# Performance work log

Measured on AMD Instinct MI355X. Metric: run time of the kernel, lower is better.

Reference implementation:

```python
import jax, jax.numpy as jnp
import numpy as np

D = 256   # dim = vis_dim = key_channels = value_channels = audio_dim
BT = 64   # batch*time
H = 64
W = 64
L = 32    # audio length

_CONV_NAMES = ["vis_project", "av", "vv", "vo", "ao", "vs_key", "vs_q1", "vs_q2",
               "as_key", "as_q1", "as_q2", "outconv", "aoc"]


def _conv1(x, w, b):
    # pointwise Conv1d: x [B,C,Lx], w [O,C], b [O]
    return jnp.einsum('oc,bcl->bol', w, x) + b[None, :, None]


def _inorm(x, eps=1e-5):
    # InstanceNorm1d (affine=False): normalize over last (spatial) axis
    m = jnp.mean(x, axis=-1, keepdims=True)
    v = jnp.var(x, axis=-1, keepdims=True)
    return (x - m) * jax.lax.rsqrt(v + eps)


def _gelu(x):
    return jax.nn.gelu(x, approximate=False)


def setup_inputs() -> dict:
    key = jax.random.key(0)
    ks = jax.random.split(key, 40)
    inp = {
        "x": jax.random.normal(ks[0], (BT, D, H, W), jnp.float32),
        "audio": jax.random.normal(ks[1], (BT, D, L), jnp.float32),
        "audio_mask": jnp.ones((BT, L, 1), jnp.float32),
    }
    for i, n in enumerate(_CONV_NAMES):
        inp[n + "_w"] = jax.random.normal(ks[3 + 2 * i], (D, D), jnp.float32) * 0.05
        inp[n + "_b"] = jax.random.normal(ks[4 + 2 * i], (D,), jnp.float32) * 0.01
    inp["gate_w1"] = jax.random.normal(ks[30], (D, D), jnp.float32) * 0.05
    inp["gate_w2"] = jax.random.normal(ks[31], (D, D), jnp.float32) * 0.05
    inp["vis_weight"] = jnp.ones((1,), jnp.float32)
    inp["audio_weight"] = jnp.ones((1,), jnp.float32)
    return inp


def reference(x, audio, audio_mask,
              vis_project_w, vis_project_b, av_w, av_b, vv_w, vv_b, vo_w, vo_b,
              ao_w, ao_b, vs_key_w, vs_key_b, vs_q1_w, vs_q1_b, vs_q2_w, vs_q2_b,
              as_key_w, as_key_b, as_q1_w, as_q1_b, as_q2_w, as_q2_b,
              outconv_w, outconv_b, aoc_w, aoc_b, gate_w1, gate_w2,
              vis_weight, audio_weight):
    bt, c, h, w = x.shape
    hw = h * w
    xf = x.reshape(bt, c, hw)                       # [BT,C,HW] (channels-first tokens)
    scale = float(D) ** -0.5                         # key_channels ** -0.5
    maskT = jnp.swapaxes(audio_mask, 1, 2)           # [BT,1,L]

    # vis_project (Conv1d 1x1 + GELU)
    vis = _gelu(_conv1(xf, vis_project_w, vis_project_b))       # [BT,C,HW]

    # ---- AV_Interaction ----
    audio_value = _conv1(audio, av_w, av_b) * maskT              # [BT,C,L]

    # Visual_Sim (kernel=1 -> unfold is identity)
    q1 = _inorm(_conv1(xf, vs_q1_w, vs_q1_b))                    # [BT,C,HW]
    q = _inorm(_conv1(q1, vs_q2_w, vs_q2_b))                     # [BT,C,HW]
    k = _conv1(audio, vs_key_w, vs_key_b) * maskT                # [BT,C,L]
    sim_v = jnp.einsum('bch,bcl->bhl', q, k) * scale             # [BT,HW,L]
    sim_v = sim_v + (10000.0 * maskT - 10000.0)                  # mask keys
    sim_v = jax.nn.softmax(sim_v, axis=-1)
    vw = jax.nn.softmax(vis_weight)[0]                           # softmax over size-1 -> 1.0
    vis_out = jnp.einsum('bhl,bcl->bhc', sim_v * vw, audio_value)  # [BT,HW,C]
    vis_out = _inorm(_conv1(jnp.swapaxes(vis_out, 1, 2), vo_w, vo_b))  # [BT,C,HW]

    # Audio_Sim (kernel=(1,1) -> pad/unfold identity)
    aq = _conv1(_conv1(audio, as_q1_w, as_q1_b), as_q2_w, as_q2_b)  # [BT,C,L]
    ak = _inorm(_conv1(xf, as_key_w, as_key_b))                     # [BT,C,HW]
    aqT = jnp.swapaxes(aq, 1, 2) * audio_mask                       # [BT,L,C]
    sim_a = jnp.einsum('blc,bch->blh', aqT, ak) * scale             # [BT,L,HW]
    sim_a = sim_a + (10000.0 * audio_mask - 10000.0)                # mask query rows
    sim_a = jax.nn.softmax(sim_a, axis=-1)
    aw = jax.nn.softmax(audio_weight)[0]
    vis_value = _inorm(_conv1(xf, vv_w, vv_b))                      # [BT,C,HW]
    audio_o = jnp.einsum('blh,bch->blc', sim_a * aw, vis_value)     # [BT,L,C]
    audio_res = _conv1(jnp.swapaxes(audio_o, 1, 2), ao_w, ao_b)     # [BT,C,L]

    # ---- Dual fusion: vis * vis_weight_map, out_conv ----
    vis = _gelu(_conv1(vis * vis_out, outconv_w, outconv_b))        # [BT,C,HW]
    vis_res = jnp.swapaxes(vis, 1, 2)                               # [BT,HW,C]

    # ---- DAM block: gated residual + audio residual ----
    gate = jnp.tanh(jax.nn.relu(vis_res @ gate_w1.T) @ gate_w2.T)   # [BT,HW,C]
    x_tok = jnp.swapaxes(xf, 1, 2) + gate * vis_res                 # [BT,HW,C]
    x_out = jnp.swapaxes(x_tok, 1, 2).reshape(bt, c, h, w)
    audio_out = audio + _gelu(_conv1(audio_res, aoc_w, aoc_b))      # [BT,C,L]
    return (x_out, audio_out)
```

## Files before the change

### kernel.cpp

```cpp
#include <hip/hip_runtime.h>
#include <math.h>

#define BT 64
#define CH 256
#define HW 4096
#define AL 32
#define SCALE 0.0625f

typedef unsigned short ushort_t;
typedef __bf16 bf16x8 __attribute__((ext_vector_type(8)));
typedef short  short8 __attribute__((ext_vector_type(8)));
typedef float  f32x4  __attribute__((ext_vector_type(4)));

__device__ __forceinline__ float gelu_f(float x){
    return 0.5f*x*(1.0f+erff(x*0.70710678118654752f));
}
__device__ __forceinline__ ushort_t f2bf(float f){
    unsigned int u = __builtin_bit_cast(unsigned int, f);
    u += 0x7fffu + ((u>>16)&1u);
    return (ushort_t)(u>>16);
}
__device__ __forceinline__ float bf2f(ushort_t h){
    unsigned int u = ((unsigned int)h)<<16;
    return __builtin_bit_cast(float, u);
}

#define GLOAD_LDS16(gp, lp) __builtin_amdgcn_global_load_lds( \
    (const __attribute__((address_space(1))) unsigned int*)(gp), \
    (__attribute__((address_space(3))) unsigned int*)(lp), 16, 0, 0)

template<int EPI, int TOUT>
__global__ __launch_bounds__(256,2)
void gemm_mfma_kernel(const ushort_t* __restrict__ Wb, const float* __restrict__ bias,
                      const ushort_t* __restrict__ Xt, float* __restrict__ Out,
                      ushort_t* __restrict__ OutB,
                      const float* __restrict__ E1, const float* __restrict__ E2)
{
    __shared__ ushort_t sW[128*32];
    __shared__ ushort_t sX[128*32];
    const int b  = blockIdx.z;
    const int o0 = blockIdx.y*128, p0 = blockIdx.x*128;
    const int tid = threadIdx.x, lane = tid & 63, w = tid >> 6;
    const int wm = w >> 1, wn = w & 1;
    const int rr = lane >> 2;
    const int kk8 = (lane & 3) * 8;

    f32x4 acc[4][4] = {};

    for (int k0 = 0; k0 < CH; k0 += 32) {
        #pragma unroll
        for (int j = 0; j < 2; ++j) {
            const ushort_t* gw = Wb + (size_t)(o0 + w*32 + j*16 + rr)*CH + k0 + kk8;
            GLOAD_LDS16(gw, sW + (size_t)w*1024 + j*512);
        }
        #pragma unroll
        for (int j = 0; j < 2; ++j) {
            const ushort_t* gx = Xt + ((size_t)b*HW + p0 + w*32 + j*16 + rr)*CH + k0 + kk8;
            GLOAD_LDS16(gx, sX + (size_t)w*1024 + j*512);
        }
        __syncthreads();
        bf16x8 af[4], bfr[4];
        #pragma unroll
        for (int mt = 0; mt < 4; ++mt) {
            short8 raw = *(const short8*)(sW + (size_t)(wm*64 + mt*16 + (lane&15))*32 + (lane>>4)*8);
            af[mt] = __builtin_bit_cast(bf16x8, raw);
        }
        #pragma unroll
        for (int nt = 0; nt < 4; ++nt) {
            short8 raw = *(const short8*)(sX + (size_t)(wn*64 + nt*16 + (lane&15))*32 + (lane>>4)*8);
            bfr[nt] = __builtin_bit_cast(bf16x8, raw);
        }
        #pragma unroll
        for (int mt = 0; mt < 4; ++mt)
            #pragma unroll
            for (int nt = 0; nt < 4; ++nt)
                acc[mt][nt] = __builtin_amdgcn_mfma_f32_16x16x32_bf16(af[mt], bfr[nt], acc[mt][nt], 0, 0, 0);
        __syncthreads();
    }

    const int pcol = lane & 15, quad = lane >> 4;
    const size_t obase = (size_t)b*CH*HW;
    if (TOUT == 0) {
        #pragma unroll
        for (int mt = 0; mt < 4; ++mt) {
            #pragma unroll
            for (int r = 0; r < 4; ++r) {
                const int o = o0 + wm*64 + mt*16 + quad*4 + r;
                const float bv = bias ? bias[o] : 0.0f;
                #pragma unroll
                for (int nt = 0; nt < 4; ++nt) {
                    const int p = p0 + wn*64 + nt*16 + pcol;
                    float v = acc[mt][nt][r] + bv;
                    if (EPI == 1) v = gelu_f(v);
                    if (EPI == 2) v = fmaxf(v, 0.0f);
                    if (EPI == 3) {
                        const size_t idx = obase + (size_t)o*HW + p;
                        v = E1[idx] + tanhf(v)*E2[idx];
                    }
                    Out[obase + (size_t)o*HW + p] = v;
                }
            }
        }
    } else {
        #pragma unroll
        for (int mt = 0; mt < 4; ++mt) {
            const int ob = o0 + wm*64 + mt*16 + quad*4;
            #pragma unroll
            for (int nt = 0; nt < 4; ++nt) {
                const int p = p0 + wn*64 + nt*16 + pcol;
                ushort4 u;
                float v0 = acc[mt][nt][0] + (bias ? bias[ob+0] : 0.f);
                float v1 = acc[mt][nt][1] + (bias ? bias[ob+1] : 0.f);
                float v2 = acc[mt][nt][2] + (bias ? bias[ob+2] : 0.f);
                float v3 = acc[mt][nt][3] + (bias ? bias[ob+3] : 0.f);
                if (EPI == 1) { v0=gelu_f(v0); v1=gelu_f(v1); v2=gelu_f(v2); v3=gelu_f(v3); }
                if (EPI == 2) { v0=fmaxf(v0,0.f); v1=fmaxf(v1,0.f); v2=fmaxf(v2,0.f); v3=fmaxf(v3,0.f); }
                u.x=f2bf(v0); u.y=f2bf(v1); u.z=f2bf(v2); u.w=f2bf(v3);
                *(ushort4*)(OutB + ((size_t)b*HW + p)*CH + ob) = u;
            }
        }
    }
}

template<int MODE>
__global__ __launch_bounds__(256)
void transpose_bf16_kernel(const float* __restrict__ Xa, const ushort_t* __restrict__ Mul,
                           ushort_t* __restrict__ Out)
{
    __shared__ float sT[32][33];
    const int b = blockIdx.z, c0 = blockIdx.y*32, p0 = blockIdx.x*32;
    const int tid = threadIdx.x;
    {
        const int cr = tid >> 3, pq = (tid & 7)*4;
        const float4 v = *(const float4*)(Xa + ((size_t)b*CH + c0 + cr)*HW + p0 + pq);
        sT[cr][pq+0]=v.x; sT[cr][pq+1]=v.y; sT[cr][pq+2]=v.z; sT[cr][pq+3]=v.w;
    }
    __syncthreads();
    {
        const int pr = tid >> 3, cq = (tid & 7)*4;
        const size_t oidx = ((size_t)b*HW + p0 + pr)*CH + c0 + cq;
        float v0 = sT[cq+0][pr], v1 = sT[cq+1][pr], v2 = sT[cq+2][pr], v3 = sT[cq+3][pr];
        if (MODE == 1) {
            const ushort4 m = *(const ushort4*)(Mul + oidx);
            v0 *= bf2f(m.x); v1 *= bf2f(m.y); v2 *= bf2f(m.z); v3 *= bf2f(m.w);
        }
        ushort4 u; u.x=f2bf(v0); u.y=f2bf(v1); u.z=f2bf(v2); u.w=f2bf(v3);
        *(ushort4*)(Out + oidx) = u;
    }
}

__global__ __launch_bounds__(256)
void wconv_kernel(const float* w0, const float* w1, const float* w2, const float* w3,
                  const float* w4, const float* w5, const float* w6, const float* w7,
                  const float* w8, ushort_t* __restrict__ Wb)
{
    const float* src;
    switch (blockIdx.y) {
        case 0: src=w0; break; case 1: src=w1; break; case 2: src=w2; break;
        case 3: src=w3; break; case 4: src=w4; break; case 5: src=w5; break;
        case 6: src=w6; break; case 7: src=w7; break; default: src=w8; break;
    }
    const int i = (blockIdx.x*256 + threadIdx.x)*4;
    const float4 v = *(const float4*)(src + i);
    ushort4 u; u.x=f2bf(v.x); u.y=f2bf(v.y); u.z=f2bf(v.z); u.w=f2bf(v.w);
    *(ushort4*)(Wb + (size_t)blockIdx.y*65536 + i) = u;
}

__global__ __launch_bounds__(256)
void inorm_hw_kernel(float* __restrict__ Buf)
{
    const size_t base = (size_t)blockIdx.x * HW;
    const int tid = threadIdx.x;
    float4 v[4];
    float s=0.f, ss=0.f;
    #pragma unroll
    for (int i=0;i<4;++i){
        v[i] = *(const float4*)(Buf + base + tid*4 + i*1024);
        s  += v[i].x+v[i].y+v[i].z+v[i].w;
        ss += v[i].x*v[i].x + v[i].y*v[i].y + v[i].z*v[i].z + v[i].w*v[i].w;
    }
    #pragma unroll
    for (int off=1; off<64; off<<=1){
        s  += __shfl_xor(s, off);
        ss += __shfl_xor(ss, off);
    }
    __shared__ float rs[4], rss[4];
    if ((tid&63)==0){ rs[tid>>6]=s; rss[tid>>6]=ss; }
    __syncthreads();
    s  = rs[0]+rs[1]+rs[2]+rs[3];
    ss = rss[0]+rss[1]+rss[2]+rss[3];
    const float mean = s * (1.0f/HW);
    const float var  = ss * (1.0f/HW) - mean*mean;
    const float r = rsqrtf(var + 1e-5f);
    #pragma unroll
    for (int i=0;i<4;++i){
        float4 t;
        t.x=(v[i].x-mean)*r; t.y=(v[i].y-mean)*r; t.z=(v[i].z-mean)*r; t.w=(v[i].w-mean)*r;
        *(float4*)(Buf + base + tid*4 + i*1024) = t;
    }
}

template<int EPI>
__global__ __launch_bounds__(256)
void conv_l_kernel(const float* __restrict__ W, const float* __restrict__ bias,
                   const float* __restrict__ X, float* __restrict__ Out,
                   const float* __restrict__ Mask, const float* __restrict__ Resid)
{
    const int b = blockIdx.x;
    const int o = blockIdx.y*8 + (threadIdx.x>>5);
    const int l = threadIdx.x & 31;
    const float* xb = X + (size_t)b*CH*AL + l;
    const float* wr = W + (size_t)o*CH;
    float acc = bias ? bias[o] : 0.0f;
    #pragma unroll 8
    for (int c=0;c<CH;++c) acc = fmaf(wr[c], xb[(size_t)c*AL], acc);
    const size_t oi = (size_t)b*CH*AL + (size_t)o*AL + l;
    if (EPI==1) acc *= Mask[b*AL + l];
    if (EPI==2) acc = Resid[oi] + gelu_f(acc);
    Out[oi] = acc;
}

__global__ __launch_bounds__(256)
void attn_v_kernel(const float* __restrict__ Q, const float* __restrict__ K,
                   const float* __restrict__ AV, const float* __restrict__ Mask,
                   float* __restrict__ Out)
{
    __shared__ float smem[12288];
    __shared__ float sBias[32];
    const int b  = blockIdx.y;
    const int p0 = blockIdx.x * 64;
    const int tid = threadIdx.x;
    const int p = tid & 63, lg = tid >> 6;

    {
        const float* kb = K + (size_t)b*CH*AL;
        #pragma unroll
        for (int i=0;i<32;++i) smem[tid + 256*i] = kb[tid + 256*i];
        if (tid < 32) sBias[tid] = 10000.f*Mask[b*AL+tid] - 10000.f;
    }
    float s[8] = {0.f,0.f,0.f,0.f,0.f,0.f,0.f,0.f};
    const float* qb = Q + (size_t)b*CH*HW + p0;
    for (int c0=0; c0<CH; c0+=64){
        __syncthreads();
        #pragma unroll
        for (int i=0;i<4;++i){
            const int cc = (tid>>4) + 16*i;
            const int pp = (tid&15)*4;
            *(float4*)&smem[8192 + cc*64 + pp] = *(const float4*)(qb + (size_t)(c0+cc)*HW + pp);
        }
        __syncthreads();
        for (int cc=0; cc<64; ++cc){
            const float qv = smem[8192 + cc*64 + p];
            const float* kr = &smem[(c0+cc)*32 + lg*8];
            #pragma unroll
            for (int j=0;j<8;++j) s[j] = fmaf(qv, kr[j], s[j]);
        }
    }
    __syncthreads();
    #pragma unroll
    for (int j=0;j<8;++j) smem[8192 + p*33 + lg*8 + j] = s[j]*SCALE + sBias[lg*8+j];
    {
        const float* avb = AV + (size_t)b*CH*AL;
        #pragma unroll
        for (int i=0;i<32;++i) smem[tid + 256*i] = avb[tid + 256*i];
    }
    __syncthreads();
    if (tid < 64){
        float* row = &smem[8192 + tid*33];
        float m = row[0];
        #pragma unroll
        for (int l=1;l<32;++l) m = fmaxf(m, row[l]);
        float z = 0.f;
        #pragma unroll
        for (int l=0;l<32;++l){ const float e = expf(row[l]-m); row[l]=e; z+=e; }
        const float rz = 1.f/z;
        #pragma unroll
        for (int l=0;l<32;++l) row[l] *= rz;
    }
    __syncthreads();
    float w[32];
    #pragma unroll
    for (int l=0;l<32;++l) w[l] = smem[8192 + p*33 + l];
    float* ob = Out + (size_t)b*CH*HW + p0 + p;
    for (int ci=0; ci<64; ++ci){
        const int c = lg*64 + ci;
        const float* ar = &smem[c*32];
        float acc = 0.f;
        #pragma unroll
        for (int l=0;l<32;++l) acc = fmaf(w[l], ar[l], acc);
        ob[(size_t)c*HW] = acc;
    }
}

__global__ __launch_bounds__(256)
void sima_raw_kernel(const float* __restrict__ AQ, const float* __restrict__ AK,
                     const float* __restrict__ Mask, float* __restrict__ Sraw)
{
    __shared__ float sAQ[CH*AL];
    const int b = blockIdx.y;
    const int p = blockIdx.x*256 + threadIdx.x;
    const int tid = threadIdx.x;
    #pragma unroll
    for (int i=0;i<32;++i){
        const int idx = tid + 256*i;
        sAQ[idx] = AQ[(size_t)b*CH*AL + idx] * Mask[b*AL + (idx&31)] * SCALE;
    }
    __syncthreads();
    float s[32];
    #pragma unroll
    for (int l=0;l<32;++l) s[l]=0.f;
    const float* akb = AK + (size_t)b*CH*HW + p;
    for (int c=0;c<CH;++c){
        const float a = akb[(size_t)c*HW];
        const float* qr = &sAQ[c*32];
        #pragma unroll
        for (int l=0;l<32;++l) s[l] = fmaf(qr[l], a, s[l]);
    }
    float* outp = Sraw + (size_t)b*AL*HW + p;
    #pragma unroll
    for (int l=0;l<32;++l) outp[(size_t)l*HW] = s[l];
}

__global__ __launch_bounds__(256)
void sima_stats_kernel(const float* __restrict__ Sraw, float2* __restrict__ Stats)
{
    const size_t base = (size_t)blockIdx.x * HW;
    const int tid = threadIdx.x;
    float v[16];
    #pragma unroll
    for (int i=0;i<4;++i){
        const float4 t = *(const float4*)(Sraw + base + tid*4 + i*1024);
        v[i*4+0]=t.x; v[i*4+1]=t.y; v[i*4+2]=t.z; v[i*4+3]=t.w;
    }
    float m = v[0];
    #pragma unroll
    for (int i=1;i<16;++i) m = fmaxf(m, v[i]);
    #pragma unroll
    for (int off=1; off<64; off<<=1) m = fmaxf(m, __shfl_xor(m, off));
    __shared__ float rm[4], rz[4];
    if ((tid&63)==0) rm[tid>>6]=m;
    __syncthreads();
    m = fmaxf(fmaxf(rm[0],rm[1]), fmaxf(rm[2],rm[3]));
    float z=0.f;
    #pragma unroll
    for (int i=0;i<16;++i) z += expf(v[i]-m);
    #pragma unroll
    for (int off=1; off<64; off<<=1) z += __shfl_xor(z, off);
    if ((tid&63)==0) rz[tid>>6]=z;
    __syncthreads();
    if (tid==0) Stats[blockIdx.x] = make_float2(m, 1.0f/(rz[0]+rz[1]+rz[2]+rz[3]));
}

__global__ __launch_bounds__(256)
void sima_pv_kernel(const float* __restrict__ Sraw, const float2* __restrict__ Stats,
                    const float* __restrict__ VV, float* __restrict__ AO)
{
    __shared__ float sA[32*33];
    __shared__ float sB[64*36];
    __shared__ float sM[32], sR[32];
    const int b  = blockIdx.x >> 2;
    const int c0 = (blockIdx.x & 3) * 64;
    const int tid = threadIdx.x;
    if (tid < 32){
        const float2 st = Stats[b*AL + tid];
        sM[tid] = st.x; sR[tid] = st.y;
    }
    __syncthreads();
    const int lh = tid & 15;
    const int cq = tid >> 4;
    const int lr = tid >> 3, k4 = (tid & 7) * 4;
    float acc[2][4] = {{0.f,0.f,0.f,0.f},{0.f,0.f,0.f,0.f}};
    for (int p0=0; p0<HW; p0+=32){
        {
            const float4 t = *(const float4*)(Sraw + ((size_t)b*AL + lr)*HW + p0 + k4);
            const float mm = sM[lr], rr2 = sR[lr];
            sA[lr*33 + k4+0] = expf(t.x-mm)*rr2;
            sA[lr*33 + k4+1] = expf(t.y-mm)*rr2;
            sA[lr*33 + k4+2] = expf(t.z-mm)*rr2;
            sA[lr*33 + k4+3] = expf(t.w-mm)*rr2;
        }
        #pragma unroll
        for (int i=0;i<2;++i){
            const int cc = (tid>>3) + 32*i;
            *(float4*)&sB[cc*36 + k4] = *(const float4*)(VV + ((size_t)b*CH + c0 + cc)*HW + p0 + k4);
        }
        __syncthreads();
        #pragma unroll
        for (int kk=0;kk<32;++kk){
            const float a0 = sA[lh*33 + kk];
            const float a1 = sA[(lh+16)*33 + kk];
            #pragma unroll
            for (int j=0;j<4;++j){
                const float bb = sB[(cq*4+j)*36 + kk];
                acc[0][j] = fmaf(a0, bb, acc[0][j]);
                acc[1][j] = fmaf(a1, bb, acc[1][j]);
            }
        }
        __syncthreads();
    }
    #pragma unroll
    for (int j=0;j<4;++j){
        AO[((size_t)b*CH + c0 + cq*4 + j)*AL + lh]      = acc[0][j];
        AO[((size_t)b*CH + c0 + cq*4 + j)*AL + lh + 16] = acc[1][j];
    }
}

extern "C" void kernel_launch(void* const* d_in, const int* in_sizes, int n_in,
                              void* d_out, int out_size, void* d_ws, size_t ws_size,
                              hipStream_t stream)
{
    (void)in_sizes; (void)n_in; (void)out_size; (void)ws_size;
    const float* x     = (const float*)d_in[0];
    const float* audio = (const float*)d_in[1];
    const float* amask = (const float*)d_in[2];
    const float* vis_project_w = (const float*)d_in[3];
    const float* vis_project_b = (const float*)d_in[4];
    const float* av_w = (const float*)d_in[5];
    const float* av_b = (const float*)d_in[6];
    const float* vv_w = (const float*)d_in[7];
    const float* vv_b = (const float*)d_in[8];
    const float* vo_w = (const float*)d_in[9];
    const float* vo_b = (const float*)d_in[10];
    const float* ao_w = (const float*)d_in[11];
    const float* ao_b = (const float*)d_in[12];
    const float* vs_key_w = (const float*)d_in[13];
    const float* vs_key_b = (const float*)d_in[14];
    const float* vs_q1_w = (const float*)d_in[15];
    const float* vs_q1_b = (const float*)d_in[16];
    const float* vs_q2_w = (const float*)d_in[17];
    const float* vs_q2_b = (const float*)d_in[18];
    const float* as_key_w = (const float*)d_in[19];
    const float* as_key_b = (const float*)d_in[20];
    const float* as_q1_w = (const float*)d_in[21];
    const float* as_q1_b = (const float*)d_in[22];
    const float* as_q2_w = (const float*)d_in[23];
    const float* as_q2_b = (const float*)d_in[24];
    const float* outconv_w = (const float*)d_in[25];
    const float* outconv_b = (const float*)d_in[26];
    const float* aoc_w = (const float*)d_in[27];
    const float* aoc_b = (const float*)d_in[28];
    const float* gate_w1 = (const float*)d_in[29];
    const float* gate_w2 = (const float*)d_in[30];

    float* out_x = (float*)d_out;
    float* out_a = out_x + (size_t)BT*CH*HW;
    float* B     = out_x;

    const size_t BIG = (size_t)BT*CH*HW;
    ushort_t* Xt   = (ushort_t*)d_ws;
    ushort_t* VISB = Xt + BIG;
    float*  A     = (float*)(VISB + BIG);
    float*  SIMA  = A + BIG;
    float2* STATS = (float2*)(SIMA + (size_t)BT*AL*HW);
    float*  S0 = (float*)(STATS + BT*AL);
    float*  S1 = S0 + (size_t)BT*CH*AL;
    float*  S2 = S1 + (size_t)BT*CH*AL;
    float*  S3 = S2 + (size_t)BT*CH*AL;
    float*  S4 = S3 + (size_t)BT*CH*AL;
    ushort_t* Wb = (ushort_t*)(S4 + (size_t)BT*CH*AL);

    dim3 b256(256);
    dim3 gW(64, 9);
    dim3 gL(BT, CH/8);
    dim3 gT(HW/32, CH/32, BT);
    dim3 gG(HW/128, CH/128, BT);
    dim3 gNorm(BT*CH);
    dim3 gAttnV(HW/64, BT);
    dim3 gSimA(HW/256, BT);

    #define WSLOT(i) (Wb + (size_t)(i)*65536)
    hipLaunchKernelGGL(wconv_kernel, gW, b256, 0, stream,
                       vs_q1_w, as_key_w, vv_w, vis_project_w, vs_q2_w, vo_w, outconv_w, gate_w1, gate_w2, Wb);
    hipLaunchKernelGGL((conv_l_kernel<1>), gL, b256, 0, stream, av_w, av_b, audio, S0, amask, nullptr);
    hipLaunchKernelGGL((conv_l_kernel<1>), gL, b256, 0, stream, vs_key_w, vs_key_b, audio, S1, amask, nullptr);
    hipLaunchKernelGGL((conv_l_kernel<0>), gL, b256, 0, stream, as_q1_w, as_q1_b, audio, S3, nullptr, nullptr);
    hipLaunchKernelGGL((conv_l_kernel<0>), gL, b256, 0, stream, as_q2_w, as_q2_b, S3, S2, nullptr, nullptr);
    hipLaunchKernelGGL((transpose_bf16_kernel<0>), gT, b256, 0, stream, x, nullptr, Xt);
    hipLaunchKernelGGL((gemm_mfma_kernel<0,0>), gG, b256, 0, stream, WSLOT(0), vs_q1_b, Xt, A, nullptr, nullptr, nullptr);
    hipLaunchKernelGGL(inorm_hw_kernel, gNorm, b256, 0, stream, A);
    hipLaunchKernelGGL((gemm_mfma_kernel<0,0>), gG, b256, 0, stream, WSLOT(1), as_key_b, Xt, B, nullptr, nullptr, nullptr);
    hipLaunchKernelGGL(inorm_hw_kernel, gNorm, b256, 0, stream, B);
    hipLaunchKernelGGL(sima_raw_kernel, gSimA, b256, 0, stream, S2, B, amask, SIMA);
    hipLaunchKernelGGL(sima_stats_kernel, dim3(BT*AL), b256, 0, stream, SIMA, STATS);
    hipLaunchKernelGGL((gemm_mfma_kernel<0,0>), gG, b256, 0, stream, WSLOT(2), vv_b, Xt, B, nullptr, nullptr, nullptr);
    hipLaunchKernelGGL(inorm_hw_kernel, gNorm, b256, 0, stream, B);
    hipLaunchKernelGGL(sima_pv_kernel, dim3(BT*4), b256, 0, stream, SIMA, STATS, B, S4);
    hipLaunchKernelGGL((conv_l_kernel<0>), gL, b256, 0, stream, ao_w, ao_b, S4, S3, nullptr, nullptr);
    hipLaunchKernelGGL((conv_l_kernel<2>), gL, b256, 0, stream, aoc_w, aoc_b, S3, out_a, nullptr, audio);
    hipLaunchKernelGGL((gemm_mfma_kernel<1,1>), gG, b256, 0, stream, WSLOT(3), vis_project_b, Xt, nullptr, VISB, nullptr, nullptr);
    hipLaunchKernelGGL((transpose_bf16_kernel<0>), gT, b256, 0, stream, A, nullptr, Xt);
    hipLaunchKernelGGL((gemm_mfma_kernel<0,0>), gG, b256, 0, stream, WSLOT(4), vs_q2_b, Xt, B, nullptr, nullptr, nullptr);
    hipLaunchKernelGGL(inorm_hw_kernel, gNorm, b256, 0, stream, B);
    hipLaunchKernelGGL(attn_v_kernel, gAttnV, b256, 0, stream, B, S1, S0, amask, A);
    hipLaunchKernelGGL((transpose_bf16_kernel<0>), gT, b256, 0, stream, A, nullptr, Xt);
    hipLaunchKernelGGL((gemm_mfma_kernel<0,0>), gG, b256, 0, stream, WSLOT(5), vo_b, Xt, B, nullptr, nullptr, nullptr);
    hipLaunchKernelGGL(inorm_hw_kernel, gNorm, b256, 0, stream, B);
    hipLaunchKernelGGL((transpose_bf16_kernel<1>), gT, b256, 0, stream, B, VISB, Xt);
    hipLaunchKernelGGL((gemm_mfma_kernel<1,0>), gG, b256, 0, stream, WSLOT(6), outconv_b, Xt, A, nullptr, nullptr, nullptr);
    hipLaunchKernelGGL((transpose_bf16_kernel<0>), gT, b256, 0, stream, A, nullptr, Xt);
    hipLaunchKernelGGL((gemm_mfma_kernel<2,0>), gG, b256, 0, stream, WSLOT(7), nullptr, Xt, B, nullptr, nullptr, nullptr);
    hipLaunchKernelGGL((transpose_bf16_kernel<0>), gT, b256, 0, stream, B, nullptr, Xt);
    hipLaunchKernelGGL((gemm_mfma_kernel<3,0>), gG, b256, 0, stream, WSLOT(8), nullptr, Xt, out_x, nullptr, x, A);
    #undef WSLOT
}
```

Measured before the change: 3.315 ms.

## Fuse instance-norm statistics into GEMM epilogues and fold normalization into consumers

```diff
diff --git a/kernel.cpp b/kernel.cpp
--- a/kernel.cpp
+++ b/kernel.cpp
@@ -29,12 +29,13 @@
     (const __attribute__((address_space(1))) unsigned int*)(gp), \
     (__attribute__((address_space(3))) unsigned int*)(lp), 16, 0, 0)
 
-template<int EPI, int TOUT>
+template<int EPI, int TOUT, int WSTAT>
 __global__ __launch_bounds__(256,2)
 void gemm_mfma_kernel(const ushort_t* __restrict__ Wb, const float* __restrict__ bias,
                       const ushort_t* __restrict__ Xt, float* __restrict__ Out,
                       ushort_t* __restrict__ OutB,
-                      const float* __restrict__ E1, const float* __restrict__ E2)
+                      const float* __restrict__ E1, const float* __restrict__ E2,
+                      float* __restrict__ St)
 {
     __shared__ ushort_t sW[128*32];
     __shared__ ushort_t sX[128*32];
@@ -101,7 +102,7 @@
                 }
             }
         }
-    } else {
+    } else if (TOUT == 1) {
         #pragma unroll
         for (int mt = 0; mt < 4; ++mt) {
             const int ob = o0 + wm*64 + mt*16 + quad*4;
@@ -119,20 +120,110 @@
                 *(ushort4*)(OutB + ((size_t)b*HW + p)*CH + ob) = u;
             }
         }
-    }
+    } else {
+        #pragma unroll
+        for (int mt = 0; mt < 4; ++mt) {
+            const int ob = o0 + wm*64 + mt*16 + quad*4;
+            #pragma unroll
+            for (int nt = 0; nt < 4; ++nt) {
+                const int p = p0 + wn*64 + nt*16 + pcol;
+                float v[4];
+                #pragma unroll
+                for (int r = 0; r < 4; ++r) {
+                    float t = acc[mt][nt][r] + (bias ? bias[ob+r] : 0.f);
+                    if (EPI == 1) t = gelu_f(t);
+                    if (EPI == 2) t = fmaxf(t, 0.f);
+                    v[r] = t;
+                    Out[obase + (size_t)(ob+r)*HW + p] = t;
+                }
+                ushort4 u;
+                u.x=f2bf(v[0]); u.y=f2bf(v[1]); u.z=f2bf(v[2]); u.w=f2bf(v[3]);
+                *(ushort4*)(OutB + ((size_t)b*HW + p)*CH + ob) = u;
+            }
+        }
+    }
+
+    if (WSTAT) {
+        float s1[4][4], s2[4][4];
+        #pragma unroll
+        for (int mt = 0; mt < 4; ++mt) {
+            #pragma unroll
+            for (int r = 0; r < 4; ++r) {
+                const int o = o0 + wm*64 + mt*16 + quad*4 + r;
+                const float bv = bias ? bias[o] : 0.0f;
+                float a = 0.f, q = 0.f;
+                #pragma unroll
+                for (int nt = 0; nt < 4; ++nt) {
+                    const float v = acc[mt][nt][r] + bv;
+                    a += v; q += v*v;
+                }
+                #pragma unroll
+                for (int off = 1; off < 16; off <<= 1) {
+                    a += __shfl_xor(a, off);
+                    q += __shfl_xor(q, off);
+                }
+                s1[mt][r] = a; s2[mt][r] = q;
+            }
+        }
+        float* red = (float*)sW;
+        __syncthreads();
+        if (wn == 0 && pcol == 0) {
+            #pragma unroll
+            for (int mt = 0; mt < 4; ++mt)
+                #pragma unroll
+                for (int r = 0; r < 4; ++r) {
+                    const int ol = wm*64 + mt*16 + quad*4 + r;
+                    red[ol*2] = s1[mt][r]; red[ol*2+1] = s2[mt][r];
+                }
+        }
+        __syncthreads();
+        if (wn == 1 && pcol == 0) {
+            #pragma unroll
+            for (int mt = 0; mt < 4; ++mt)
+                #pragma unroll
+                for (int r = 0; r < 4; ++r) {
+                    const int ol = wm*64 + mt*16 + quad*4 + r;
+                    const int o = o0 + ol;
+                    atomicAdd(&St[((size_t)b*CH + o)*2],   red[ol*2]   + s1[mt][r]);
+                    atomicAdd(&St[((size_t)b*CH + o)*2+1], red[ol*2+1] + s2[mt][r]);
+                }
+        }
+    }
+}
+
+__global__ __launch_bounds__(256)
+void zero_kernel(float* __restrict__ p)
+{
+    p[blockIdx.x*256 + threadIdx.x] = 0.f;
+}
+
+__global__ __launch_bounds__(256)
+void stats_finalize_kernel(float* __restrict__ St)
+{
+    const int row = blockIdx.x*256 + threadIdx.x;
+    const float s1 = St[(size_t)row*2], s2 = St[(size_t)row*2+1];
+    const float mean = s1 * (1.0f/HW);
+    const float var  = s2 * (1.0f/HW) - mean*mean;
+    St[(size_t)row*2]   = mean;
+    St[(size_t)row*2+1] = rsqrtf(var + 1e-5f);
 }
 
 template<int MODE>
 __global__ __launch_bounds__(256)
 void transpose_bf16_kernel(const float* __restrict__ Xa, const ushort_t* __restrict__ Mul,
-                           ushort_t* __restrict__ Out)
+                           const float* __restrict__ St, ushort_t* __restrict__ Out)
 {
     __shared__ float sT[32][33];
     const int b = blockIdx.z, c0 = blockIdx.y*32, p0 = blockIdx.x*32;
     const int tid = threadIdx.x;
     {
         const int cr = tid >> 3, pq = (tid & 7)*4;
-        const float4 v = *(const float4*)(Xa + ((size_t)b*CH + c0 + cr)*HW + p0 + pq);
+        float4 v = *(const float4*)(Xa + ((size_t)b*CH + c0 + cr)*HW + p0 + pq);
+        if (MODE >= 1) {
+            const float m = St[((size_t)b*CH + c0 + cr)*2];
+            const float r = St[((size_t)b*CH + c0 + cr)*2+1];
+            v.x = (v.x-m)*r; v.y = (v.y-m)*r; v.z = (v.z-m)*r; v.w = (v.w-m)*r;
+        }
         sT[cr][pq+0]=v.x; sT[cr][pq+1]=v.y; sT[cr][pq+2]=v.z; sT[cr][pq+3]=v.w;
     }
     __syncthreads();
@@ -140,7 +231,7 @@
         const int pr = tid >> 3, cq = (tid & 7)*4;
         const size_t oidx = ((size_t)b*HW + p0 + pr)*CH + c0 + cq;
         float v0 = sT[cq+0][pr], v1 = sT[cq+1][pr], v2 = sT[cq+2][pr], v3 = sT[cq+3][pr];
-        if (MODE == 1) {
+        if (MODE == 2) {
             const ushort4 m = *(const ushort4*)(Mul + oidx);
             v0 *= bf2f(m.x); v1 *= bf2f(m.y); v2 *= bf2f(m.z); v3 *= bf2f(m.w);
         }
@@ -166,45 +257,12 @@
     *(ushort4*)(Wb + (size_t)blockIdx.y*65536 + i) = u;
 }
 
-__global__ __launch_bounds__(256)
-void inorm_hw_kernel(float* __restrict__ Buf)
-{
-    const size_t base = (size_t)blockIdx.x * HW;
-    const int tid = threadIdx.x;
-    float4 v[4];
-    float s=0.f, ss=0.f;
-    #pragma unroll
-    for (int i=0;i<4;++i){
-        v[i] = *(const float4*)(Buf + base + tid*4 + i*1024);
-        s  += v[i].x+v[i].y+v[i].z+v[i].w;
-        ss += v[i].x*v[i].x + v[i].y*v[i].y + v[i].z*v[i].z + v[i].w*v[i].w;
-    }
-    #pragma unroll
-    for (int off=1; off<64; off<<=1){
-        s  += __shfl_xor(s, off);
-        ss += __shfl_xor(ss, off);
-    }
-    __shared__ float rs[4], rss[4];
-    if ((tid&63)==0){ rs[tid>>6]=s; rss[tid>>6]=ss; }
-    __syncthreads();
-    s  = rs[0]+rs[1]+rs[2]+rs[3];
-    ss = rss[0]+rss[1]+rss[2]+rss[3];
-    const float mean = s * (1.0f/HW);
-    const float var  = ss * (1.0f/HW) - mean*mean;
-    const float r = rsqrtf(var + 1e-5f);
-    #pragma unroll
-    for (int i=0;i<4;++i){
-        float4 t;
-        t.x=(v[i].x-mean)*r; t.y=(v[i].y-mean)*r; t.z=(v[i].z-mean)*r; t.w=(v[i].w-mean)*r;
-        *(float4*)(Buf + base + tid*4 + i*1024) = t;
-    }
-}
-
-template<int EPI>
+template<int EPI, int TR>
 __global__ __launch_bounds__(256)
 void conv_l_kernel(const float* __restrict__ W, const float* __restrict__ bias,
                    const float* __restrict__ X, float* __restrict__ Out,
-                   const float* __restrict__ Mask, const float* __restrict__ Resid)
+                   const float* __restrict__ Mask, const float* __restrict__ Resid,
+                   const float* __restrict__ St)
 {
     const int b = blockIdx.x;
     const int o = blockIdx.y*8 + (threadIdx.x>>5);
@@ -214,87 +272,154 @@
     float acc = bias ? bias[o] : 0.0f;
     #pragma unroll 8
     for (int c=0;c<CH;++c) acc = fmaf(wr[c], xb[(size_t)c*AL], acc);
-    const size_t oi = (size_t)b*CH*AL + (size_t)o*AL + l;
     if (EPI==1) acc *= Mask[b*AL + l];
-    if (EPI==2) acc = Resid[oi] + gelu_f(acc);
-    Out[oi] = acc;
-}
-
-__global__ __launch_bounds__(256)
-void attn_v_kernel(const float* __restrict__ Q, const float* __restrict__ K,
-                   const float* __restrict__ AV, const float* __restrict__ Mask,
-                   float* __restrict__ Out)
-{
-    __shared__ float smem[12288];
+    if (EPI==4) acc *= Mask[b*AL + l] * St[((size_t)b*CH + o)*2+1] * SCALE;
+    if (EPI==2) {
+        const size_t oi = (size_t)b*CH*AL + (size_t)o*AL + l;
+        acc = Resid[oi] + gelu_f(acc);
+    }
+    if (TR == 0) Out[(size_t)b*CH*AL + (size_t)o*AL + l] = acc;
+    else         Out[((size_t)b*AL + l)*CH + o] = acc;
+}
+
+__global__ __launch_bounds__(256)
+void lbias_kernel(const float* __restrict__ Kn, const float* __restrict__ St,
+                  float* __restrict__ Lb)
+{
+    const int b = blockIdx.x, tid = threadIdx.x;
+    const int l = tid & 31, g = tid >> 5;
+    float s = 0.f;
+    #pragma unroll 8
+    for (int cc=0; cc<32; ++cc){
+        const int c = g*32 + cc;
+        s += St[((size_t)b*CH + c)*2] * Kn[((size_t)b*CH + c)*AL + l];
+    }
+    __shared__ float red[8][32];
+    red[g][l] = s;
+    __syncthreads();
+    if (tid < 32){
+        float t = 0.f;
+        #pragma unroll
+        for (int gg=0; gg<8; ++gg) t += red[gg][tid];
+        Lb[b*AL + tid] = -t;
+    }
+}
+
+__device__ __forceinline__ void attn_loadq(f32x4 (&dst)[8], const float* Qb, int kc){
+    #pragma unroll
+    for (int kk=0;kk<8;++kk)
+        dst[kk] = *(const f32x4*)(Qb + (size_t)(kc*8+kk)*HW);
+}
+__device__ __forceinline__ void attn_fma(float (&s)[4][4], const f32x4 (&q)[8],
+                                         const float* sKV, int kc, int lq){
+    #pragma unroll
+    for (int kk=0;kk<8;++kk){
+        const f32x4 kv = *(const f32x4*)&sKV[(kc*8+kk)*32 + lq*4];
+        #pragma unroll
+        for (int i=0;i<4;++i)
+            #pragma unroll
+            for (int j=0;j<4;++j)
+                s[i][j] = fmaf(q[kk][i], kv[j], s[i][j]);
+    }
+}
+
+__global__ __launch_bounds__(256,3)
+void attn_v_kernel(const float* __restrict__ Q, const float* __restrict__ Kn,
+                   const float* __restrict__ AVt, const float* __restrict__ Lb,
+                   const float* __restrict__ Mask, ushort_t* __restrict__ OutB)
+{
+    __shared__ float sKV[8192];
+    __shared__ float sP[32*128];
     __shared__ float sBias[32];
     const int b  = blockIdx.y;
-    const int p0 = blockIdx.x * 64;
+    const int p0 = blockIdx.x * 128;
     const int tid = threadIdx.x;
-    const int p = tid & 63, lg = tid >> 6;
-
+    const int pg = tid >> 3;
+    const int lq = tid & 7;
+
+    #pragma unroll
+    for (int ii=0; ii<8; ++ii){
+        const int fi = ii*256 + tid;
+        *(f32x4*)&sKV[fi*4] = *(const f32x4*)(Kn + (size_t)b*CH*AL + (size_t)fi*4);
+    }
+    if (tid < 32) sBias[tid] = Lb[b*AL + tid] + 10000.f*Mask[b*AL + tid] - 10000.f;
+    __syncthreads();
+
+    const float* Qb = Q + (size_t)b*CH*HW + p0 + pg*4;
+    float s[4][4] = {};
     {
-        const float* kb = K + (size_t)b*CH*AL;
-        #pragma unroll
-        for (int i=0;i<32;++i) smem[tid + 256*i] = kb[tid + 256*i];
-        if (tid < 32) sBias[tid] = 10000.f*Mask[b*AL+tid] - 10000.f;
-    }
-    float s[8] = {0.f,0.f,0.f,0.f,0.f,0.f,0.f,0.f};
-    const float* qb = Q + (size_t)b*CH*HW + p0;
+        f32x4 qa[8], qb2[8];
+        attn_loadq(qa, Qb, 0);
+        for (int kc = 0; kc < 32; kc += 2){
+            attn_loadq(qb2, Qb, kc+1);
+            attn_fma(s, qa, sKV, kc, lq);
+            if (kc+2 < 32) attn_loadq(qa, Qb, kc+2);
+            attn_fma(s, qb2, sKV, kc+1, lq);
+        }
+    }
+    __syncthreads();
+
+    #pragma unroll
+    for (int j=0;j<4;++j)
+        *(f32x4*)&sP[(lq*4+j)*128 + pg*4] = (f32x4){s[0][j], s[1][j], s[2][j], s[3][j]};
+    #pragma unroll
+    for (int ii=0; ii<8; ++ii){
+        const int fi = ii*256 + tid;
+        *(f32x4*)&sKV[fi*4] = *(const f32x4*)(AVt + (size_t)b*AL*CH + (size_t)fi*4);
+    }
+    __syncthreads();
+
+    {
+        const int p = tid >> 1, lh = tid & 1;
+        float v[16];
+        #pragma unroll
+        for (int jj=0;jj<16;++jj) v[jj] = sP[(lh*16+jj)*128 + p] + sBias[lh*16+jj];
+        float m = v[0];
+        #pragma unroll
+        for (int jj=1;jj<16;++jj) m = fmaxf(m, v[jj]);
+        m = fmaxf(m, __shfl_xor(m, 1));
+        float z = 0.f;
+        #pragma unroll
+        for (int jj=0;jj<16;++jj){ v[jj] = expf(v[jj]-m); z += v[jj]; }
+        z += __shfl_xor(z, 1);
+        const float rz = 1.f/z;
+        #pragma unroll
+        for (int jj=0;jj<16;++jj) sP[(lh*16+jj)*128 + p] = v[jj]*rz;
+    }
+    __syncthreads();
+
+    const int cg = lq;
+    ushort_t* Ob = OutB + ((size_t)b*HW + p0 + pg*4)*CH;
+    #pragma unroll 1
     for (int c0=0; c0<CH; c0+=64){
-        __syncthreads();
+        float acc[4][8] = {};
+        #pragma unroll
+        for (int k=0;k<32;++k){
+            const f32x4 pv = *(const f32x4*)&sP[k*128 + pg*4];
+            const f32x4 a0 = *(const f32x4*)&sKV[k*256 + c0 + cg*8];
+            const f32x4 a1 = *(const f32x4*)&sKV[k*256 + c0 + cg*8 + 4];
+            #pragma unroll
+            for (int i=0;i<4;++i){
+                acc[i][0]=fmaf(pv[i],a0[0],acc[i][0]); acc[i][1]=fmaf(pv[i],a0[1],acc[i][1]);
+                acc[i][2]=fmaf(pv[i],a0[2],acc[i][2]); acc[i][3]=fmaf(pv[i],a0[3],acc[i][3]);
+                acc[i][4]=fmaf(pv[i],a1[0],acc[i][4]); acc[i][5]=fmaf(pv[i],a1[1],acc[i][5]);
+                acc[i][6]=fmaf(pv[i],a1[2],acc[i][6]); acc[i][7]=fmaf(pv[i],a1[3],acc[i][7]);
+            }
+        }
         #pragma unroll
         for (int i=0;i<4;++i){
-            const int cc = (tid>>4) + 16*i;
-            const int pp = (tid&15)*4;
-            *(float4*)&smem[8192 + cc*64 + pp] = *(const float4*)(qb + (size_t)(c0+cc)*HW + pp);
-        }
-        __syncthreads();
-        for (int cc=0; cc<64; ++cc){
-            const float qv = smem[8192 + cc*64 + p];
-            const float* kr = &smem[(c0+cc)*32 + lg*8];
-            #pragma unroll
-            for (int j=0;j<8;++j) s[j] = fmaf(qv, kr[j], s[j]);
-        }
-    }
-    __syncthreads();
-    #pragma unroll
-    for (int j=0;j<8;++j) smem[8192 + p*33 + lg*8 + j] = s[j]*SCALE + sBias[lg*8+j];
-    {
-        const float* avb = AV + (size_t)b*CH*AL;
-        #pragma unroll
-        for (int i=0;i<32;++i) smem[tid + 256*i] = avb[tid + 256*i];
-    }
-    __syncthreads();
-    if (tid < 64){
-        float* row = &smem[8192 + tid*33];
-        float m = row[0];
-        #pragma unroll
-        for (int l=1;l<32;++l) m = fmaxf(m, row[l]);
-        float z = 0.f;
-        #pragma unroll
-        for (int l=0;l<32;++l){ const float e = expf(row[l]-m); row[l]=e; z+=e; }
-        const float rz = 1.f/z;
-        #pragma unroll
-        for (int l=0;l<32;++l) row[l] *= rz;
-    }
-    __syncthreads();
-    float w[32];
-    #pragma unroll
-    for (int l=0;l<32;++l) w[l] = smem[8192 + p*33 + l];
-    float* ob = Out + (size_t)b*CH*HW + p0 + p;
-    for (int ci=0; ci<64; ++ci){
-        const int c = lg*64 + ci;
-        const float* ar = &smem[c*32];
-        float acc = 0.f;
-        #pragma unroll
-        for (int l=0;l<32;++l) acc = fmaf(w[l], ar[l], acc);
-        ob[(size_t)c*HW] = acc;
+            short8 u;
+            #pragma unroll
+            for (int j=0;j<8;++j) u[j] = (short)f2bf(acc[i][j]);
+            *(short8*)(Ob + (size_t)i*CH + c0 + cg*8) = u;
+        }
     }
 }
 
 __global__ __launch_bounds__(256)
 void sima_raw_kernel(const float* __restrict__ AQ, const float* __restrict__ AK,
-                     const float* __restrict__ Mask, float* __restrict__ Sraw)
+                     const float* __restrict__ Mask, const float* __restrict__ St,
+                     float* __restrict__ Sraw)
 {
     __shared__ float sAQ[CH*AL];
     const int b = blockIdx.y;
@@ -303,7 +428,8 @@
     #pragma unroll
     for (int i=0;i<32;++i){
         const int idx = tid + 256*i;
-        sAQ[idx] = AQ[(size_t)b*CH*AL + idx] * Mask[b*AL + (idx&31)] * SCALE;
+        sAQ[idx] = AQ[(size_t)b*CH*AL + idx] * Mask[b*AL + (idx&31)] * SCALE
+                 * St[((size_t)b*CH + (idx>>5))*2+1];
     }
     __syncthreads();
     float s[32];
@@ -352,8 +478,9 @@
 }
 
 __global__ __launch_bounds__(256)
-void sima_pv_kernel(const float* __restrict__ Sraw, const float2* __restrict__ Stats,
-                    const float* __restrict__ VV, float* __restrict__ AO)
+void sima_pv_kernel(const float* __restrict__ Sraw, const float2* __restrict__ SmStats,
+                    const float* __restrict__ VV, const float* __restrict__ ChSt,
+                    float* __restrict__ AO)
 {
     __shared__ float sA[32*33];
     __shared__ float sB[64*36];
@@ -362,7 +489,7 @@
     const int c0 = (blockIdx.x & 3) * 64;
     const int tid = threadIdx.x;
     if (tid < 32){
-        const float2 st = Stats[b*AL + tid];
+        const float2 st = SmStats[b*AL + tid];
         sM[tid] = st.x; sR[tid] = st.y;
     }
     __syncthreads();
@@ -400,8 +527,11 @@
     }
     #pragma unroll
     for (int j=0;j<4;++j){
-        AO[((size_t)b*CH + c0 + cq*4 + j)*AL + lh]      = acc[0][j];
-        AO[((size_t)b*CH + c0 + cq*4 + j)*AL + lh + 16] = acc[1][j];
+        const int c = c0 + cq*4 + j;
+        const float m0 = ChSt[((size_t)b*CH + c)*2];
+        const float r0 = ChSt[((size_t)b*CH + c)*2+1];
+        AO[((size_t)b*CH + c)*AL + lh]      = (acc[0][j]-m0)*r0;
+        AO[((size_t)b*CH + c)*AL + lh + 16] = (acc[1][j]-m0)*r0;
     }
 }
 
@@ -458,48 +588,55 @@
     float*  S3 = S2 + (size_t)BT*CH*AL;
     float*  S4 = S3 + (size_t)BT*CH*AL;
     ushort_t* Wb = (ushort_t*)(S4 + (size_t)BT*CH*AL);
+    float*  SA = (float*)(Wb + (size_t)9*65536);
+    float*  SB = SA + (size_t)2*BT*CH;
+    float*  LB = SB + (size_t)2*BT*CH;
 
     dim3 b256(256);
     dim3 gW(64, 9);
     dim3 gL(BT, CH/8);
     dim3 gT(HW/32, CH/32, BT);
     dim3 gG(HW/128, CH/128, BT);
-    dim3 gNorm(BT*CH);
-    dim3 gAttnV(HW/64, BT);
+    dim3 gAttnV(HW/128, BT);
     dim3 gSimA(HW/256, BT);
+    dim3 gZ(2*BT*CH/256);
+    dim3 gF(BT*CH/256);
 
     #define WSLOT(i) (Wb + (size_t)(i)*65536)
     hipLaunchKernelGGL(wconv_kernel, gW, b256, 0, stream,
                        vs_q1_w, as_key_w, vv_w, vis_project_w, vs_q2_w, vo_w, outconv_w, gate_w1, gate_w2, Wb);
-    hipLaunchKernelGGL((conv_l_kernel<1>), gL, b256, 0, stream, av_w, av_b, audio, S0, amask, nullptr);
-    hipLaunchKernelGGL((conv_l_kernel<1>), gL, b256, 0, stream, vs_key_w, vs_key_b, audio, S1, amask, nullptr);
-    hipLaunchKernelGGL((conv_l_kernel<0>), gL, b256, 0, stream, as_q1_w, as_q1_b, audio, S3, nullptr, nullptr);
-    hipLaunchKernelGGL((conv_l_kernel<0>), gL, b256, 0, stream, as_q2_w, as_q2_b, S3, S2, nullptr, nullptr);
-    hipLaunchKernelGGL((transpose_bf16_kernel<0>), gT, b256, 0, stream, x, nullptr, Xt);
-    hipLaunchKernelGGL((gemm_mfma_kernel<0,0>), gG, b256, 0, stream, WSLOT(0), vs_q1_b, Xt, A, nullptr, nullptr, nullptr);
-    hipLaunchKernelGGL(inorm_hw_kernel, gNorm, b256, 0, stream, A);
-    hipLaunchKernelGGL((gemm_mfma_kernel<0,0>), gG, b256, 0, stream, WSLOT(1), as_key_b, Xt, B, nullptr, nullptr, nullptr);
-    hipLaunchKernelGGL(inorm_hw_kernel, gNorm, b256, 0, stream, B);
-    hipLaunchKernelGGL(sima_raw_kernel, gSimA, b256, 0, stream, S2, B, amask, SIMA);
+    hipLaunchKernelGGL((conv_l_kernel<1,1>), gL, b256, 0, stream, av_w, av_b, audio, S0, amask, nullptr, nullptr);
+    hipLaunchKernelGGL((conv_l_kernel<0,0>), gL, b256, 0, stream, as_q1_w, as_q1_b, audio, S3, nullptr, nullptr, nullptr);
+    hipLaunchKernelGGL((conv_l_kernel<0,0>), gL, b256, 0, stream, as_q2_w, as_q2_b, S3, S2, nullptr, nullptr, nullptr);
+    hipLaunchKernelGGL((transpose_bf16_kernel<0>), gT, b256, 0, stream, x, nullptr, nullptr, Xt);
+    hipLaunchKernelGGL(zero_kernel, gZ, b256, 0, stream, SA);
+    hipLaunchKernelGGL((gemm_mfma_kernel<0,0,1>), gG, b256, 0, stream, WSLOT(0), vs_q1_b, Xt, A, nullptr, nullptr, nullptr, SA);
+    hipLaunchKernelGGL(stats_finalize_kernel, gF, b256, 0, stream, SA);
+    hipLaunchKernelGGL(zero_kernel, gZ, b256, 0, stream, SB);
+    hipLaunchKernelGGL((gemm_mfma_kernel<0,0,1>), gG, b256, 0, stream, WSLOT(1), as_key_b, Xt, B, nullptr, nullptr, nullptr, SB);
+    hipLaunchKernelGGL(stats_finalize_kernel, gF, b256, 0, stream, SB);
+    hipLaunchKernelGGL(sima_raw_kernel, gSimA, b256, 0, stream, S2, B, amask, SB, SIMA);
     hipLaunchKernelGGL(sima_stats_kernel, dim3(BT*AL), b256, 0, stream, SIMA, STATS);
-    hipLaunchKernelGGL((gemm_mfma_kernel<0,0>), gG, b256, 0, stream, WSLOT(2), vv_b, Xt, B, nullptr, nullptr, nullptr);
-    hipLaunchKernelGGL(inorm_hw_kernel, gNorm, b256, 0, stream, B);
-    hipLaunchKernelGGL(sima_pv_kernel, dim3(BT*4), b256, 0, stream, SIMA, STATS, B, S4);
-    hipLaunchKernelGGL((conv_l_kernel<0>), gL, b256, 0, stream, ao_w, ao_b, S4, S3, nullptr, nullptr);
-    hipLaunchKernelGGL((conv_l_kernel<2>), gL, b256, 0, stream, aoc_w, aoc_b, S3, out_a, nullptr, audio);
-    hipLaunchKernelGGL((gemm_mfma_kernel<1,1>), gG, b256, 0, stream, WSLOT(3), vis_project_b, Xt, nullptr, VISB, nullptr, nullptr);
-    hipLaunchKernelGGL((transpose_bf16_kernel<0>), gT, b256, 0, stream, A, nullptr, Xt);
-    hipLaunchKernelGGL((gemm_mfma_kernel<0,0>), gG, b256, 0, stream, WSLOT(4), vs_q2_b, Xt, B, nullptr, nullptr, nullptr);
-    hipLaunchKernelGGL(inorm_hw_kernel, gNorm, b256, 0, stream, B);
-    hipLaunchKernelGGL(attn_v_kernel, gAttnV, b256, 0, stream, B, S1, S0, amask, A);
-    hipLaunchKernelGGL((transpose_bf16_kernel<0>), gT, b256, 0, stream, A, nullptr, Xt);
-    hipLaunchKernelGGL((gemm_mfma_kernel<0,0>), gG, b256, 0, stream, WSLOT(5), vo_b, Xt, B, nullptr, nullptr, nullptr);
-    hipLaunchKernelGGL(inorm_hw_kernel, gNorm, b256, 0, stream, B);
-    hipLaunchKernelGGL((transpose_bf16_kernel<1>), gT, b256, 0, stream, B, VISB, Xt);
-    hipLaunchKernelGGL((gemm_mfma_kernel<1,0>), gG, b256, 0, stream, WSLOT(6), outconv_b, Xt, A, nullptr, nullptr, nullptr);
-    hipLaunchKernelGGL((transpose_bf16_kernel<0>), gT, b256, 0, stream, A, nullptr, Xt);
-    hipLaunchKernelGGL((gemm_mfma_kernel<2,0>), gG, b256, 0, stream, WSLOT(7), nullptr, Xt, B, nullptr, nullptr, nullptr);
-    hipLaunchKernelGGL((transpose_bf16_kernel<0>), gT, b256, 0, stream, B, nullptr, Xt);
-    hipLaunchKernelGGL((gemm_mfma_kernel<3,0>), gG, b256, 0, stream, WSLOT(8), nullptr, Xt, out_x, nullptr, x, A);
+    hipLaunchKernelGGL(zero_kernel, gZ, b256, 0, stream, SB);
+    hipLaunchKernelGGL((gemm_mfma_kernel<0,0,1>), gG, b256, 0, stream, WSLOT(2), vv_b, Xt, B, nullptr, nullptr, nullptr, SB);
+    hipLaunchKernelGGL(stats_finalize_kernel, gF, b256, 0, stream, SB);
+    hipLaunchKernelGGL(sima_pv_kernel, dim3(BT*4), b256, 0, stream, SIMA, STATS, B, SB, S4);
+    hipLaunchKernelGGL((conv_l_kernel<0,0>), gL, b256, 0, stream, ao_w, ao_b, S4, S3, nullptr, nullptr, nullptr);
+    hipLaunchKernelGGL((conv_l_kernel<2,0>), gL, b256, 0, stream, aoc_w, aoc_b, S3, out_a, nullptr, audio, nullptr);
+    hipLaunchKernelGGL((gemm_mfma_kernel<1,1,0>), gG, b256, 0, stream, WSLOT(3), vis_project_b, Xt, nullptr, VISB, nullptr, nullptr, nullptr);
+    hipLaunchKernelGGL((transpose_bf16_kernel<1>), gT, b256, 0, stream, A, nullptr, SA, Xt);
+    hipLaunchKernelGGL(zero_kernel, gZ, b256, 0, stream, SA);
+    hipLaunchKernelGGL((gemm_mfma_kernel<0,0,1>), gG, b256, 0, stream, WSLOT(4), vs_q2_b, Xt, B, nullptr, nullptr, nullptr, SA);
+    hipLaunchKernelGGL(stats_finalize_kernel, gF, b256, 0, stream, SA);
+    hipLaunchKernelGGL((conv_l_kernel<4,0>), gL, b256, 0, stream, vs_key_w, vs_key_b, audio, S1, amask, nullptr, SA);
+    hipLaunchKernelGGL(lbias_kernel, dim3(BT), b256, 0, stream, S1, SA, LB);
+    hipLaunchKernelGGL(attn_v_kernel, gAttnV, b256, 0, stream, B, S1, S0, LB, amask, Xt);
+    hipLaunchKernelGGL(zero_kernel, gZ, b256, 0, stream, SA);
+    hipLaunchKernelGGL((gemm_mfma_kernel<0,0,1>), gG, b256, 0, stream, WSLOT(5), vo_b, Xt, B, nullptr, nullptr, nullptr, SA);
+    hipLaunchKernelGGL(stats_finalize_kernel, gF, b256, 0, stream, SA);
+    hipLaunchKernelGGL((transpose_bf16_kernel<2>), gT, b256, 0, stream, B, VISB, SA, Xt);
+    hipLaunchKernelGGL((gemm_mfma_kernel<1,2,0>), gG, b256, 0, stream, WSLOT(6), outconv_b, Xt, A, VISB, nullptr, nullptr, nullptr);
+    hipLaunchKernelGGL((gemm_mfma_kernel<2,1,0>), gG, b256, 0, stream, WSLOT(7), nullptr, VISB, nullptr, Xt, nullptr, nullptr, nullptr);
+    hipLaunchKernelGGL((gemm_mfma_kernel<3,0,0>), gG, b256, 0, stream, WSLOT(8), nullptr, Xt, out_x, nullptr, x, A, nullptr);
     #undef WSLOT
 }
```

After: 2.954 ms. 10.9% less time.
